# Performance work log

Measured on AMD Instinct MI355X. Metric: run time of the kernel, lower is better.

Reference implementation:

```python
import jax, jax.numpy as jnp
import numpy as np

B, N, C = 2048, 64, 384
H, WS, HIDDEN, TEMB = 12, 8, 64, 384
D = C // H


def _rpb_index(ws):
    coords = np.stack(np.meshgrid(np.arange(ws), np.arange(ws), indexing='ij'))  # (2, ws, ws)
    flat = coords.reshape(2, -1)                       # (2, ws*ws)
    rel = flat[:, :, None] - flat[:, None, :]          # (2, N, N)
    rel = rel.transpose(1, 2, 0).copy()                # (N, N, 2)
    rel[..., 0] += ws - 1
    rel[..., 1] += ws - 1
    rel[..., 0] *= 2 * ws - 1
    return rel.sum(-1)                                  # (N, N) int


def setup_inputs() -> dict:
    key = jax.random.key(0)
    ks = jax.random.split(key, 16)
    s = 0.02
    inp = {
        'x': jax.random.normal(ks[0], (B, N, C), jnp.float32),
        'temb': jax.random.normal(ks[1], (B, TEMB), jnp.float32),
        'sigma': jax.random.uniform(ks[2], (B,), jnp.float32, 1e-3, 1.0),
        'qkv_w': jax.random.normal(ks[3], (C, 3 * C), jnp.float32) * s,
        'qkv_b': jax.random.normal(ks[4], (3 * C,), jnp.float32) * s,
        'qkvt_w': jax.random.normal(ks[5], (TEMB, 3 * C), jnp.float32) * s,
        'trunk_w1': jax.random.normal(ks[6], (1, HIDDEN), jnp.float32) * s,
        'trunk_b1': jax.random.normal(ks[7], (HIDDEN,), jnp.float32) * s,
        'trunk_w2': jax.random.normal(ks[8], (HIDDEN, HIDDEN), jnp.float32) * s,
        'trunk_b2': jax.random.normal(ks[9], (HIDDEN,), jnp.float32) * s,
        'gate_w': jax.random.normal(ks[10], (HIDDEN, 1), jnp.float32) * s,
        'gate_b': jnp.zeros((1,), jnp.float32),
        'bias_w': jax.random.normal(ks[11], (HIDDEN, H), jnp.float32) * s,
        'bias_b': jax.random.normal(ks[12], (H,), jnp.float32) * s,
        'proj_w': jax.random.normal(ks[13], (C, C), jnp.float32) * s,
        'proj_b': jax.random.normal(ks[14], (C,), jnp.float32) * s,
        'rpb_table': jax.random.normal(ks[15], ((2 * WS - 1) * (2 * WS - 1), H), jnp.float32) * s,
        'rpb_index': jnp.asarray(_rpb_index(WS), jnp.int32),
    }
    return inp


def reference(x, temb, sigma, qkv_w, qkv_b, qkvt_w, trunk_w1, trunk_b1,
              trunk_w2, trunk_b2, gate_w, gate_b, bias_w, bias_b,
              proj_w, proj_b, rpb_table, rpb_index):
    b, n, c = x.shape
    h, d = H, c // H
    scale = d ** -0.5
    # QKV with time-embedding modulation
    qkv = x @ qkv_w + qkv_b + (temb @ qkvt_w)[:, None, :]        # (B, N, 3C)
    qkv = qkv.reshape(b, n, 3, h, d).transpose(2, 0, 3, 1, 4)     # (3, B, H, N, D)
    q, k, v = qkv[0], qkv[1], qkv[2]
    attn = jnp.einsum('bhnd,bhmd->bhnm', q * scale, k)            # (B, H, N, N)
    # relative position bias
    rpb = rpb_table[rpb_index].transpose(2, 0, 1)                 # (H, N, N)
    attn = attn + rpb[None]
    # noise-conditioned gate and per-head bias
    log_sigma = jnp.log(jnp.clip(sigma, 1e-6))[:, None]           # (B, 1)
    hid = jax.nn.silu(log_sigma @ trunk_w1 + trunk_b1)
    hid = jax.nn.silu(hid @ trunk_w2 + trunk_b2)                  # (B, hidden)
    gate = jax.nn.sigmoid(hid @ gate_w + gate_b).reshape(b, 1, 1, 1)
    nbias = (hid @ bias_w + bias_b).reshape(b, h, 1, 1)
    attn = attn / (1.0 + gate) + nbias
    attn = jax.nn.softmax(attn, axis=-1)
    out = jnp.einsum('bhnm,bhmd->bhnd', attn, v)                  # (B, H, N, D)
    out = out.transpose(0, 2, 1, 3).reshape(b, n, c)
    return out @ proj_w + proj_b
```

## Files before the change

kernel.cpp:

```cpp
#include <hip/hip_runtime.h>
#include <hip/hip_bf16.h>

#define B_TOT 2048
#define SEQ 64
#define CH 384
#define NH 12
#define HD 32
#define NC3 1152
#define LDP 392
#define QKS 40
#define VS 72
#define HDSZ 7424
#define QK_SCALE 0.17677669529663687f

typedef __attribute__((ext_vector_type(8))) short short8;
typedef __attribute__((ext_vector_type(4))) short short4v;
typedef __attribute__((ext_vector_type(4))) float f32x4;
typedef unsigned short u16;

__device__ __forceinline__ u16 f2bf(float f) {
  __hip_bfloat16 h = __float2bfloat16(f);
  return *reinterpret_cast<u16*>(&h);
}
__device__ __forceinline__ float bf2f(u16 u) {
  return __uint_as_float(((unsigned int)u) << 16);
}

__device__ __forceinline__ int pswz(int row, int col) {
  return row * 64 + ((((col >> 3) ^ (row & 7)) << 3) | (col & 7));
}

__global__ __launch_bounds__(256) void k_aux(
    const float* __restrict__ qkv_w, const float* __restrict__ proj_w,
    const float* __restrict__ rpb_table, const int* __restrict__ rpb_index,
    const float* __restrict__ sigma, const float* __restrict__ w1,
    const float* __restrict__ b1, const float* __restrict__ w2,
    const float* __restrict__ b2, const float* __restrict__ gw,
    const float* __restrict__ gb, const float* __restrict__ bw,
    const float* __restrict__ bb, const float* __restrict__ temb,
    const float* __restrict__ qkvt_w, const float* __restrict__ qkv_b,
    u16* __restrict__ qkvwt, u16* __restrict__ projwt, u16* __restrict__ rpbz,
    float* __restrict__ inv1pg, float* __restrict__ nbias, float* __restrict__ tvec)
{
  __shared__ float shmem[16 * 384];
  const int bid = blockIdx.x;
  const int tid = threadIdx.x;

  if (bid < 2496) {
    int idx = bid * 256 + tid;
    if (idx < CH * NC3) {
      int k = idx / NC3, n = idx - k * NC3;
      qkvwt[n * LDP + k] = f2bf(qkv_w[idx]);
      return;
    }
    idx -= CH * NC3;
    if (idx < CH * CH) {
      int k = idx / CH, n = idx - k * CH;
      projwt[n * LDP + k] = f2bf(proj_w[idx]);
      return;
    }
    idx -= CH * CH;
    if (idx < NH * SEQ * SEQ) {
      int h = idx >> 12, j = (idx >> 6) & 63, q = idx & 63;
      int jt = j >> 4, g4j = (j >> 2) & 3, r = j & 3;
      int qt = q >> 4, q16 = q & 15;
      int dst = (h * 16 + jt * 4 + qt) * 256 + g4j * 64 + q16 * 4 + r;
      rpbz[dst] = f2bf(rpb_table[rpb_index[q * 64 + j] * NH + h]);
    }
    return;
  }
  if (bid < 3008) {
    float* sh = shmem;
    const int bt = tid >> 6, j = tid & 63;
    const int b = (bid - 2496) * 4 + bt;
    float ls = logf(fmaxf(sigma[b], 1e-6f));
    float z = fmaf(ls, w1[j], b1[j]);
    z = z / (1.f + __expf(-z));
    sh[bt * 64 + j] = z;
    __syncthreads();
    float a = b2[j];
    #pragma unroll 8
    for (int i = 0; i < 64; ++i) a = fmaf(sh[bt * 64 + i], w2[i * 64 + j], a);
    a = a / (1.f + __expf(-a));
    __syncthreads();
    sh[bt * 64 + j] = a;
    __syncthreads();
    if (j == 0) {
      float zg = gb[0];
      #pragma unroll 8
      for (int i = 0; i < 64; ++i) zg = fmaf(sh[bt * 64 + i], gw[i], zg);
      float gate = 1.f / (1.f + __expf(-zg));
      inv1pg[b] = 1.f / (1.f + gate);
    }
    if (j < NH) {
      float zb = bb[j];
      #pragma unroll 8
      for (int i = 0; i < 64; ++i) zb = fmaf(sh[bt * 64 + i], bw[i * NH + j], zb);
      nbias[b * NH + j] = zb;
    }
    return;
  }
  {
    const int bi = bid - 3008;
    const int brow = bi / 9, cseg = bi - brow * 9;
    const int cb = cseg * 128;
    for (int idx = tid; idx < 16 * 384; idx += 256) {
      int r = idx / 384, k = idx - r * 384;
      shmem[idx] = temb[(brow * 16 + r) * 384 + k];
    }
    __syncthreads();
    int cl = tid & 127, half = tid >> 7;
    float acc[8];
    #pragma unroll
    for (int i = 0; i < 8; ++i) acc[i] = 0.f;
    #pragma unroll 4
    for (int k = 0; k < 384; ++k) {
      float w = qkvt_w[k * NC3 + cb + cl];
      #pragma unroll
      for (int i = 0; i < 8; ++i) acc[i] = fmaf(shmem[(half * 8 + i) * 384 + k], w, acc[i]);
    }
    float qb = qkv_b[cb + cl];
    #pragma unroll
    for (int i = 0; i < 8; ++i)
      tvec[(brow * 16 + half * 8 + i) * NC3 + cb + cl] = acc[i] + qb;
  }
}

template<int NT>
__device__ __forceinline__ void gemm_qkv(f32x4 (&acc)[8][2],
                                         const u16* __restrict__ sx,
                                         const u16* __restrict__ qkvwt,
                                         int g, int nt0, int q16, int g4)
{
  const f32x4 fz = {0.f, 0.f, 0.f, 0.f};
  const u16* bp[NT];
  #pragma unroll
  for (int i = 0; i < NT; ++i) {
    int nt = nt0 + i;
    int hj = nt / 6, wi = nt - hj * 6;
    int mh = wi >> 1, hf = wi & 1;
    int c = mh * CH + (g * 2 + hj) * HD + hf * 16 + q16;
    bp[i] = qkvwt + c * LDP + g4 * 8;
  }
  #pragma unroll
  for (int m = 0; m < 8; ++m)
    #pragma unroll
    for (int i = 0; i < NT; ++i) acc[m][i] = fz;
  #pragma unroll 2
  for (int kt = 0; kt < 12; ++kt) {
    short8 af[8];
    #pragma unroll
    for (int m = 0; m < 8; ++m)
      af[m] = *reinterpret_cast<const short8*>(&sx[(m * 16 + q16) * LDP + kt * 32 + g4 * 8]);
    #pragma unroll
    for (int i = 0; i < NT; ++i) {
      short8 bf = *reinterpret_cast<const short8*>(bp[i] + kt * 32);
      #pragma unroll
      for (int m = 0; m < 8; ++m)
        acc[m][i] = __builtin_amdgcn_mfma_f32_16x16x32_bf16(af[m], bf, acc[m][i], 0, 0, 0);
    }
  }
}

template<int NT>
__device__ __forceinline__ void epi_qkv(const f32x4 (&acc)[8][2], u16* __restrict__ shd,
                                        const float* __restrict__ tvb,
                                        int g, int nt0, int q16, int g4)
{
  #pragma unroll
  for (int i = 0; i < NT; ++i) {
    int nt = nt0 + i;
    int hj = nt / 6, wi = nt - hj * 6;
    int mh = wi >> 1, hf = wi & 1;
    int c = mh * CH + (g * 2 + hj) * HD + hf * 16 + q16;
    float tv0 = tvb[c], tv1 = tvb[NC3 + c];
    int cof = hf * 16 + q16;
    #pragma unroll
    for (int m = 0; m < 8; ++m) {
      int bt = m >> 2;
      u16* hbase = &shd[(bt * 2 + hj) * HDSZ];
      int mrow = (m & 3) * 16 + g4 * 4;
      f32x4 a = acc[m][i];
      float tvv = bt ? tv1 : tv0;
      if (mh == 0) {
        #pragma unroll
        for (int r = 0; r < 4; ++r)
          hbase[(mrow + r) * QKS + cof] = f2bf((a[r] + tvv) * QK_SCALE);
      } else if (mh == 1) {
        #pragma unroll
        for (int r = 0; r < 4; ++r)
          hbase[2560 + (mrow + r) * QKS + cof] = f2bf(a[r] + tvv);
      } else {
        short4v pk;
        #pragma unroll
        for (int r = 0; r < 4; ++r) pk[r] = (short)f2bf(a[r] + tvv);
        *reinterpret_cast<short4v*>(&hbase[5120 + cof * VS + mrow]) = pk;
      }
    }
  }
}

__global__ __launch_bounds__(512, 2) void k_attn(
    const float* __restrict__ x, const float* __restrict__ tvec,
    const float* __restrict__ inv1pg, const float* __restrict__ nbias,
    const u16* __restrict__ qkvwt, const u16* __restrict__ rpbz,
    u16* __restrict__ attw)
{
  __shared__ __align__(16) u16 s_x[128 * LDP];
  __shared__ __align__(16) u16 s_hd[4 * HDSZ];
  const f32x4 fz = {0.f, 0.f, 0.f, 0.f};

  const int b0 = blockIdx.x * 2;
  const int tid = threadIdx.x;
  const int w = tid >> 6, l = tid & 63;
  const int q16 = l & 15, g4 = l >> 4;

  {
    const float* xb = x + (size_t)b0 * (SEQ * CH);
    #pragma unroll 4
    for (int it = 0; it < 24; ++it) {
      int fi = it * 512 + tid;
      int row = fi / 96, c4 = fi - row * 96;
      const float4 a = *reinterpret_cast<const float4*>(xb + fi * 4);
      short4v v;
      v[0] = (short)f2bf(a.x); v[1] = (short)f2bf(a.y);
      v[2] = (short)f2bf(a.z); v[3] = (short)f2bf(a.w);
      *reinterpret_cast<short4v*>(&s_x[row * LDP + c4 * 4]) = v;
    }
  }
  __syncthreads();

  const float invb0 = inv1pg[b0], invb1 = inv1pg[b0 + 1];
  const float* tvb = tvec + (size_t)b0 * NC3;

  const int nt0 = (w < 4) ? 2 * w : 8 + (w - 4);

  f32x4 acc[8][2];
  if (w < 4) gemm_qkv<2>(acc, s_x, qkvwt, 0, nt0, q16, g4);
  else       gemm_qkv<1>(acc, s_x, qkvwt, 0, nt0, q16, g4);

  for (int g = 0; g < 6; ++g) {
    if (g) __syncthreads();
    if (w < 4) epi_qkv<2>(acc, s_hd, tvb, g, nt0, q16, g4);
    else       epi_qkv<1>(acc, s_hd, tvb, g, nt0, q16, g4);
    __syncthreads();

    f32x4 st2[2][4];
    #pragma unroll
    for (int t = 0; t < 2; ++t) {
      const int tau = w * 2 + t;
      const int cmb = tau >> 2, qt = tau & 3;
      const int bt = cmb >> 1, hh = cmb & 1;
      const int h = g * 2 + hh;
      const u16* sq = &s_hd[cmb * HDSZ];
      const u16* sk = sq + 2560;
      const float inv = bt ? invb1 : invb0;
      const float nb = nbias[(b0 + bt) * NH + h];

      short4v rp4[4];
      #pragma unroll
      for (int jt = 0; jt < 4; ++jt)
        rp4[jt] = *reinterpret_cast<const short4v*>(
            &rpbz[(h * 16 + jt * 4 + qt) * 256 + g4 * 64 + q16 * 4]);

      short8 bq = *reinterpret_cast<const short8*>(&sq[(qt * 16 + q16) * QKS + g4 * 8]);
      #pragma unroll
      for (int jt = 0; jt < 4; ++jt) {
        short8 ak = *reinterpret_cast<const short8*>(&sk[(jt * 16 + q16) * QKS + g4 * 8]);
        st2[t][jt] = __builtin_amdgcn_mfma_f32_16x16x32_bf16(ak, bq, fz, 0, 0, 0);
      }
      float mx = -1e30f;
      #pragma unroll
      for (int jt = 0; jt < 4; ++jt)
        #pragma unroll
        for (int r = 0; r < 4; ++r) {
          float s = fmaf(st2[t][jt][r], inv, fmaf(bf2f((u16)rp4[jt][r]), inv, nb));
          st2[t][jt][r] = s;
          mx = fmaxf(mx, s);
        }
      mx = fmaxf(mx, __shfl_xor(mx, 16));
      mx = fmaxf(mx, __shfl_xor(mx, 32));
      float sum = 0.f;
      #pragma unroll
      for (int jt = 0; jt < 4; ++jt)
        #pragma unroll
        for (int r = 0; r < 4; ++r) {
          float p = __expf(st2[t][jt][r] - mx);
          st2[t][jt][r] = p;
          sum += p;
        }
      sum += __shfl_xor(sum, 16);
      sum += __shfl_xor(sum, 32);
      float rn = 1.f / sum;
      #pragma unroll
      for (int jt = 0; jt < 4; ++jt)
        #pragma unroll
        for (int r = 0; r < 4; ++r) st2[t][jt][r] *= rn;
    }
    __syncthreads();

    if (g < 5) {
      if (w < 4) gemm_qkv<2>(acc, s_x, qkvwt, g + 1, nt0, q16, g4);
      else       gemm_qkv<1>(acc, s_x, qkvwt, g + 1, nt0, q16, g4);
    }
    #pragma unroll
    for (int t = 0; t < 2; ++t) {
      const int tau = w * 2 + t;
      const int cmb = tau >> 2, qt = tau & 3;
      const int bt = cmb >> 1, hh = cmb & 1;
      const int h = g * 2 + hh;
      u16* sq = &s_hd[cmb * HDSZ];
      const u16* svt = sq + 5120;
      u16* P = sq;

      #pragma unroll
      for (int jt = 0; jt < 4; ++jt) {
        short4v pk;
        #pragma unroll
        for (int r = 0; r < 4; ++r) pk[r] = (short)f2bf(st2[t][jt][r]);
        *reinterpret_cast<short4v*>(&P[pswz(qt * 16 + q16, jt * 16 + 4 * g4)]) = pk;
      }
      f32x4 o[2];
      o[0] = fz; o[1] = fz;
      #pragma unroll
      for (int kk = 0; kk < 2; ++kk) {
        short8 ap = *reinterpret_cast<const short8*>(
            &P[pswz(qt * 16 + q16, kk * 32 + g4 * 8)]);
        #pragma unroll
        for (int dt = 0; dt < 2; ++dt) {
          short8 bv = *reinterpret_cast<const short8*>(
              &svt[(dt * 16 + q16) * VS + kk * 32 + g4 * 8]);
          o[dt] = __builtin_amdgcn_mfma_f32_16x16x32_bf16(ap, bv, o[dt], 0, 0, 0);
        }
      }
      u16* ab = attw + (size_t)(b0 + bt) * (SEQ * CH);
      #pragma unroll
      for (int dt = 0; dt < 2; ++dt)
        #pragma unroll
        for (int r = 0; r < 4; ++r)
          ab[(qt * 16 + g4 * 4 + r) * CH + h * HD + dt * 16 + q16] = f2bf(o[dt][r]);
    }
  }
}

__global__ __launch_bounds__(512, 4) void k_proj(
    const u16* __restrict__ attw, const u16* __restrict__ projwt,
    const float* __restrict__ proj_b, float* __restrict__ out)
{
  __shared__ __align__(16) u16 s_a[64 * LDP];
  const f32x4 fz = {0.f, 0.f, 0.f, 0.f};
  const int tid = threadIdx.x;
  const int w = tid >> 6, l = tid & 63;
  const int q16 = l & 15, g4 = l >> 4;
  const size_t row0 = (size_t)blockIdx.x * 64;

  {
    const u16* ab = attw + row0 * CH;
    #pragma unroll
    for (int it = 0; it < 6; ++it) {
      int slot = it * 512 + tid;
      int row = slot / 48, c8 = slot - row * 48;
      short8 v = *reinterpret_cast<const short8*>(ab + row * CH + c8 * 8);
      *reinterpret_cast<short8*>(&s_a[row * LDP + c8 * 8]) = v;
    }
  }
  __syncthreads();

  const u16* bpw[3]; float4 pb4[3];
  #pragma unroll
  for (int i = 0; i < 3; ++i) {
    int nt = w * 3 + i;
    bpw[i] = projwt + (nt * 16 + q16) * LDP + g4 * 8;
    pb4[i] = *reinterpret_cast<const float4*>(&proj_b[nt * 16 + 4 * g4]);
  }
  f32x4 acc[4][3];
  #pragma unroll
  for (int m = 0; m < 4; ++m)
    #pragma unroll
    for (int i = 0; i < 3; ++i) acc[m][i] = fz;
  #pragma unroll 2
  for (int kt = 0; kt < 12; ++kt) {
    short8 af[4];
    #pragma unroll
    for (int m = 0; m < 4; ++m)
      af[m] = *reinterpret_cast<const short8*>(&s_a[(m * 16 + q16) * LDP + kt * 32 + g4 * 8]);
    short8 bf[3];
    #pragma unroll
    for (int i = 0; i < 3; ++i)
      bf[i] = *reinterpret_cast<const short8*>(bpw[i] + kt * 32);
    #pragma unroll
    for (int i = 0; i < 3; ++i)
      #pragma unroll
      for (int m = 0; m < 4; ++m)
        acc[m][i] = __builtin_amdgcn_mfma_f32_16x16x32_bf16(bf[i], af[m], acc[m][i], 0, 0, 0);
  }
  float* ob = out + row0 * CH;
  #pragma unroll
  for (int i = 0; i < 3; ++i) {
    int cb = (w * 3 + i) * 16 + 4 * g4;
    #pragma unroll
    for (int m = 0; m < 4; ++m) {
      float4 v;
      v.x = acc[m][i][0] + pb4[i].x;
      v.y = acc[m][i][1] + pb4[i].y;
      v.z = acc[m][i][2] + pb4[i].z;
      v.w = acc[m][i][3] + pb4[i].w;
      *reinterpret_cast<float4*>(&ob[(m * 16 + q16) * CH + cb]) = v;
    }
  }
}

extern "C" void kernel_launch(void* const* d_in, const int* in_sizes, int n_in,
                              void* d_out, int out_size, void* d_ws, size_t ws_size,
                              hipStream_t stream) {
  const float* x       = (const float*)d_in[0];
  const float* temb    = (const float*)d_in[1];
  const float* sigma   = (const float*)d_in[2];
  const float* qkv_w   = (const float*)d_in[3];
  const float* qkv_b   = (const float*)d_in[4];
  const float* qkvt_w  = (const float*)d_in[5];
  const float* w1      = (const float*)d_in[6];
  const float* b1      = (const float*)d_in[7];
  const float* w2      = (const float*)d_in[8];
  const float* b2      = (const float*)d_in[9];
  const float* gw      = (const float*)d_in[10];
  const float* gb      = (const float*)d_in[11];
  const float* bw      = (const float*)d_in[12];
  const float* bb      = (const float*)d_in[13];
  const float* proj_w  = (const float*)d_in[14];
  const float* proj_b  = (const float*)d_in[15];
  const float* rpb_tab = (const float*)d_in[16];
  const int*   rpb_idx = (const int*)d_in[17];
  float* out = (float*)d_out;

  char* ws = (char*)d_ws;
  float* tvec   = (float*)(ws);
  float* inv1pg = (float*)(ws + 9437184);
  float* nbias  = (float*)(ws + 9445376);
  u16*   qkvwt  = (u16*)  (ws + 9543680);
  u16*   projwt = (u16*)  (ws + 10446848);
  u16*   rpbz   = (u16*)  (ws + 10747904);
  u16*   attw   = (u16*)  (ws + 10846208);

  k_aux<<<4160, 256, 0, stream>>>(qkv_w, proj_w, rpb_tab, rpb_idx,
                                  sigma, w1, b1, w2, b2, gw, gb, bw, bb,
                                  temb, qkvt_w, qkv_b,
                                  qkvwt, projwt, rpbz, inv1pg, nbias, tvec);
  k_attn<<<1024, 512, 0, stream>>>(x, tvec, inv1pg, nbias, qkvwt, rpbz, attw);
  k_proj<<<2048, 512, 0, stream>>>(attw, projwt, proj_b, out);
}
```

Before: 403.9 us.

## Split next-group QKV GEMM into halves interleaved with softmax phase

The QKV GEMM for the next head group is split into two K-halves. The first half is issued before the QK^T/softmax computation and the second half after it, so MFMA work overlaps the softmax's VALU/transcendental work. The max and sum reductions in softmax are also restructured into tree form to shorten dependency chains. Holding the accumulators live across the softmax raises register pressure, which may reduce occupancy or cause spills.

New measurement: 420.9 us. 1.04x slower.

```diff
diff --git a/kernel.cpp b/kernel.cpp
--- a/kernel.cpp
+++ b/kernel.cpp
@@ -126,11 +126,11 @@
   }
 }
 
-template<int NT>
-__device__ __forceinline__ void gemm_qkv(f32x4 (&acc)[8][2],
-                                         const u16* __restrict__ sx,
-                                         const u16* __restrict__ qkvwt,
-                                         int g, int nt0, int q16, int g4)
+template<int NT, bool INIT>
+__device__ __forceinline__ void gemm_half(f32x4 (&acc)[8][2],
+                                          const u16* __restrict__ sx,
+                                          const u16* __restrict__ qkvwt,
+                                          int g, int nt0, int kt0, int q16, int g4)
 {
   const f32x4 fz = {0.f, 0.f, 0.f, 0.f};
   const u16* bp[NT];
@@ -142,12 +142,15 @@
     int c = mh * CH + (g * 2 + hj) * HD + hf * 16 + q16;
     bp[i] = qkvwt + c * LDP + g4 * 8;
   }
-  #pragma unroll
-  for (int m = 0; m < 8; ++m)
-    #pragma unroll
-    for (int i = 0; i < NT; ++i) acc[m][i] = fz;
-  #pragma unroll 2
-  for (int kt = 0; kt < 12; ++kt) {
+  if (INIT) {
+    #pragma unroll
+    for (int m = 0; m < 8; ++m)
+      #pragma unroll
+      for (int i = 0; i < NT; ++i) acc[m][i] = fz;
+  }
+  #pragma unroll
+  for (int kk = 0; kk < 6; ++kk) {
+    int kt = kt0 + kk;
     short8 af[8];
     #pragma unroll
     for (int m = 0; m < 8; ++m)
@@ -236,8 +239,13 @@
   const int nt0 = (w < 4) ? 2 * w : 8 + (w - 4);
 
   f32x4 acc[8][2];
-  if (w < 4) gemm_qkv<2>(acc, s_x, qkvwt, 0, nt0, q16, g4);
-  else       gemm_qkv<1>(acc, s_x, qkvwt, 0, nt0, q16, g4);
+  if (w < 4) {
+    gemm_half<2, true >(acc, s_x, qkvwt, 0, nt0, 0, q16, g4);
+    gemm_half<2, false>(acc, s_x, qkvwt, 0, nt0, 6, q16, g4);
+  } else {
+    gemm_half<1, true >(acc, s_x, qkvwt, 0, nt0, 0, q16, g4);
+    gemm_half<1, false>(acc, s_x, qkvwt, 0, nt0, 6, q16, g4);
+  }
 
   for (int g = 0; g < 6; ++g) {
     if (g) __syncthreads();
@@ -245,6 +253,10 @@
     else       epi_qkv<1>(acc, s_hd, tvb, g, nt0, q16, g4);
     __syncthreads();
 
+    if (g < 5) {
+      if (w < 4) gemm_half<2, true >(acc, s_x, qkvwt, g + 1, nt0, 0, q16, g4);
+      else       gemm_half<1, true >(acc, s_x, qkvwt, g + 1, nt0, 0, q16, g4);
+    }
     f32x4 st2[2][4];
     #pragma unroll
     for (int t = 0; t < 2; ++t) {
@@ -269,26 +281,27 @@
         short8 ak = *reinterpret_cast<const short8*>(&sk[(jt * 16 + q16) * QKS + g4 * 8]);
         st2[t][jt] = __builtin_amdgcn_mfma_f32_16x16x32_bf16(ak, bq, fz, 0, 0, 0);
       }
-      float mx = -1e30f;
       #pragma unroll
       for (int jt = 0; jt < 4; ++jt)
         #pragma unroll
-        for (int r = 0; r < 4; ++r) {
-          float s = fmaf(st2[t][jt][r], inv, fmaf(bf2f((u16)rp4[jt][r]), inv, nb));
-          st2[t][jt][r] = s;
-          mx = fmaxf(mx, s);
-        }
+        for (int r = 0; r < 4; ++r)
+          st2[t][jt][r] = fmaf(st2[t][jt][r], inv, fmaf(bf2f((u16)rp4[jt][r]), inv, nb));
+      float mj[4];
+      #pragma unroll
+      for (int jt = 0; jt < 4; ++jt)
+        mj[jt] = fmaxf(fmaxf(st2[t][jt][0], st2[t][jt][1]),
+                       fmaxf(st2[t][jt][2], st2[t][jt][3]));
+      float mx = fmaxf(fmaxf(mj[0], mj[1]), fmaxf(mj[2], mj[3]));
       mx = fmaxf(mx, __shfl_xor(mx, 16));
       mx = fmaxf(mx, __shfl_xor(mx, 32));
-      float sum = 0.f;
-      #pragma unroll
-      for (int jt = 0; jt < 4; ++jt)
-        #pragma unroll
-        for (int r = 0; r < 4; ++r) {
-          float p = __expf(st2[t][jt][r] - mx);
-          st2[t][jt][r] = p;
-          sum += p;
-        }
+      float sj[4];
+      #pragma unroll
+      for (int jt = 0; jt < 4; ++jt) {
+        #pragma unroll
+        for (int r = 0; r < 4; ++r) st2[t][jt][r] = __expf(st2[t][jt][r] - mx);
+        sj[jt] = (st2[t][jt][0] + st2[t][jt][1]) + (st2[t][jt][2] + st2[t][jt][3]);
+      }
+      float sum = (sj[0] + sj[1]) + (sj[2] + sj[3]);
       sum += __shfl_xor(sum, 16);
       sum += __shfl_xor(sum, 32);
       float rn = 1.f / sum;
@@ -300,8 +313,8 @@
     __syncthreads();
 
     if (g < 5) {
-      if (w < 4) gemm_qkv<2>(acc, s_x, qkvwt, g + 1, nt0, q16, g4);
-      else       gemm_qkv<1>(acc, s_x, qkvwt, g + 1, nt0, q16, g4);
+      if (w < 4) gemm_half<2, false>(acc, s_x, qkvwt, g + 1, nt0, 6, q16, g4);
+      else       gemm_half<1, false>(acc, s_x, qkvwt, g + 1, nt0, 6, q16, g4);
     }
     #pragma unroll
     for (int t = 0; t < 2; ++t) {
```
